# Kernel optimization log

Hardware: AMD Instinct MI355X
Metric: run time of the kernel (lower is better)

Reference implementation:

```python
import jax, jax.numpy as jnp
import numpy as np

N, E, D = 100000, 640000, 128  # nodes, edges, feature dim (in_dim == out_dim == 128)
BN_EPS = 1e-5


def setup_inputs() -> dict:
    key = jax.random.key(0)
    ks = jax.random.split(key, 8)
    x = jax.random.normal(ks[0], (N, D), dtype=jnp.float32)
    edge_index = jax.random.randint(ks[1], (2, E), 0, N, dtype=jnp.int64)
    s = 1.0 / np.sqrt(D)
    W1 = jax.random.uniform(ks[2], (D, D), jnp.float32, -s, s)
    b1 = jax.random.uniform(ks[3], (D,), jnp.float32, -s, s)
    W2 = jax.random.uniform(ks[4], (D, D), jnp.float32, -s, s)
    b2 = jax.random.uniform(ks[5], (D,), jnp.float32, -s, s)
    return {
        "x": x,
        "edge_index": edge_index,
        "eps": jnp.array([0.1], dtype=jnp.float32),
        "W1": W1, "b1": b1,
        "g1": jnp.ones((D,), jnp.float32), "beta1": jnp.zeros((D,), jnp.float32),
        "W2": W2, "b2": b2,
        "g2": jnp.ones((D,), jnp.float32), "beta2": jnp.zeros((D,), jnp.float32),
    }


def _batchnorm(h, gamma, beta):
    # BatchNorm1d in training mode: biased batch stats over the node dim
    mean = jnp.mean(h, axis=0)
    var = jnp.var(h, axis=0)
    return gamma * (h - mean) * jax.lax.rsqrt(var + BN_EPS) + beta


def reference(x, edge_index, eps, W1, b1, g1, beta1, W2, b2, g2, beta2):
    src, dst = edge_index[0], edge_index[1]
    # gather messages from source nodes, scatter-add into destination nodes
    aggr = jax.ops.segment_sum(x[src], dst, num_segments=x.shape[0])  # [N, D]
    h = (1.0 + eps) * x + aggr
    h = jax.nn.relu(_batchnorm(h @ W1.T + b1, g1, beta1))
    h = jax.nn.relu(_batchnorm(h @ W2.T + b2, g2, beta2))
    return h
```

## Files before the change

kernel.cpp:

```cpp
#include <hip/hip_runtime.h>

#define NN 100000
#define DD 128
#define EE 640000
#define NPAD 100352
#define NCHUNK 391
#define NREP 8

typedef __bf16 bf16x8 __attribute__((ext_vector_type(8)));
typedef float floatx4 __attribute__((ext_vector_type(4)));

union BF8 {
    bf16x8 v;
    unsigned short u[8];
    int4 i4;
};

__device__ __forceinline__ unsigned short f2bf(float f) {
    unsigned int u = __float_as_uint(f);
    u += 0x7FFF + ((u >> 16) & 1);
    return (unsigned short)(u >> 16);
}

__device__ __forceinline__ float bf2f(unsigned short h) {
    return __uint_as_float(((unsigned int)h) << 16);
}

__global__ __launch_bounds__(256) void hist_k(const int* __restrict__ ei,
                                              int* __restrict__ degr) {
    int e = blockIdx.x * 256 + threadIdx.x;
    atomicAdd(&degr[(blockIdx.x & (NREP - 1)) * NPAD + ei[EE + e]], 1);
}

__global__ __launch_bounds__(256) void convert_k(const float4* __restrict__ x4,
                                                 ushort4* __restrict__ xbf) {
    int base = blockIdx.x * 1024 + threadIdx.x;
    float4 v0 = x4[base];
    float4 v1 = x4[base + 256];
    float4 v2 = x4[base + 512];
    float4 v3 = x4[base + 768];
    ushort4 u0, u1, u2, u3;
    u0.x = f2bf(v0.x); u0.y = f2bf(v0.y); u0.z = f2bf(v0.z); u0.w = f2bf(v0.w);
    u1.x = f2bf(v1.x); u1.y = f2bf(v1.y); u1.z = f2bf(v1.z); u1.w = f2bf(v1.w);
    u2.x = f2bf(v2.x); u2.y = f2bf(v2.y); u2.z = f2bf(v2.z); u2.w = f2bf(v2.w);
    u3.x = f2bf(v3.x); u3.y = f2bf(v3.y); u3.z = f2bf(v3.z); u3.w = f2bf(v3.w);
    xbf[base] = u0;
    xbf[base + 256] = u1;
    xbf[base + 512] = u2;
    xbf[base + 768] = u3;
}

__global__ __launch_bounds__(256) void scanlb_k(
    int* __restrict__ degr, unsigned int* __restrict__ descr,
    int* __restrict__ offs, int* __restrict__ curr) {
    __shared__ int s[256];
    __shared__ int sbase;
    const int c = blockIdx.x, t = threadIdx.x;
    int g = c * 256 + t;
    int dr[NREP];
    int v = 0;
    if (g < NN) {
#pragma unroll
        for (int r = 0; r < NREP; ++r) {
            dr[r] = degr[r * NPAD + g];
            v += dr[r];
        }
    } else {
#pragma unroll
        for (int r = 0; r < NREP; ++r) dr[r] = 0;
    }
    s[t] = v;
    __syncthreads();
    for (int off = 1; off < 256; off <<= 1) {
        int u = (t >= off) ? s[t - off] : 0;
        __syncthreads();
        s[t] += u;
        __syncthreads();
    }
    const int total = s[255];
    if (c == 0) {
        if (t == 0) {
            __hip_atomic_store(&descr[0], (2u << 30) | (unsigned)total,
                               __ATOMIC_RELEASE, __HIP_MEMORY_SCOPE_AGENT);
            sbase = 0;
        }
    } else if (t < 64) {
        if (t == 0)
            __hip_atomic_store(&descr[c], (1u << 30) | (unsigned)total,
                               __ATOMIC_RELEASE, __HIP_MEMORY_SCOPE_AGENT);
        int acc = 0;
        int base = c - 1;
        while (true) {
            int p = base - t;
            unsigned st = (p >= 0)
                ? __hip_atomic_load(&descr[p], __ATOMIC_ACQUIRE,
                                    __HIP_MEMORY_SCOPE_AGENT)
                : (2u << 30);
            unsigned fl = st >> 30;
            unsigned long long b2 = __ballot(fl == 2u);
            unsigned long long b0 = __ballot(fl == 0u);
            int l2 = b2 ? (__ffsll(b2) - 1) : 64;
            int l0 = b0 ? (__ffsll(b0) - 1) : 64;
            if (l0 < l2) continue;
            unsigned contrib = (t <= l2) ? (st & 0x3FFFFFFFu) : 0u;
#pragma unroll
            for (int o2 = 32; o2 > 0; o2 >>= 1)
                contrib += __shfl_down(contrib, o2, 64);
            contrib = __shfl(contrib, 0, 64);
            acc += (int)contrib;
            if (l2 < 64) break;
            base -= 64;
        }
        if (t == 0) {
            sbase = acc;
            __hip_atomic_store(&descr[c], (2u << 30) | (unsigned)(acc + total),
                               __ATOMIC_RELEASE, __HIP_MEMORY_SCOPE_AGENT);
        }
    }
    __syncthreads();
    if (g < NN) {
        int o = sbase + s[t] - v;
        offs[g] = o;
        int running = o;
#pragma unroll
        for (int r = 0; r < NREP; ++r) {
            curr[r * NPAD + g] = running;
            running += dr[r];
        }
        degr[g] = v;
    }
}

__global__ __launch_bounds__(256) void esort_k(
    const int* __restrict__ ei, int* __restrict__ curr,
    int* __restrict__ ssrc, const float* __restrict__ W1,
    const float* __restrict__ W2, unsigned short* __restrict__ wbf,
    float* __restrict__ stats) {
    int b = blockIdx.x;
    if (b >= 2500) {
        int i = (b - 2500) * 256 + threadIdx.x;
        if (b == 2500) {
            stats[threadIdx.x] = 0.f;
            stats[256 + threadIdx.x] = 0.f;
        }
        const float4* s4 = (i < 4096) ? (const float4*)W1 : (const float4*)W2;
        float4 v = s4[i & 4095];
        ushort4 u;
        u.x = f2bf(v.x); u.y = f2bf(v.y); u.z = f2bf(v.z); u.w = f2bf(v.w);
        ((ushort4*)wbf)[i] = u;
        return;
    }
    int e = b * 256 + threadIdx.x;
    int pos = atomicAdd(&curr[(b & (NREP - 1)) * NPAD + ei[EE + e]], 1);
    ssrc[pos] = ei[e];
}

__global__ __launch_bounds__(256, 4) void aggregate_k(
    const ushort4* __restrict__ xb, const int* __restrict__ ssrc,
    const int* __restrict__ offs, const int* __restrict__ deg,
    const float* __restrict__ epsp, ushort4* __restrict__ hout) {
    int tid = blockIdx.x * 256 + threadIdx.x;
    int node = tid >> 5, lane = tid & 31;
    if (node >= NN) return;
    int start = offs[node], d = deg[node];
    float ef = 1.0f + epsp[0];
    ushort4 ov = xb[node * 32 + lane];
    float ax = ef * bf2f(ov.x), ay = ef * bf2f(ov.y);
    float az = ef * bf2f(ov.z), aw = ef * bf2f(ov.w);
    for (int j = 0; j < d; j += 8) {
        int r = d - j;
        int b = start + j;
        int s0 = ssrc[b];
        int s1 = ssrc[b + ((r > 1) ? 1 : 0)];
        int s2 = ssrc[b + ((r > 2) ? 2 : 0)];
        int s3 = ssrc[b + ((r > 3) ? 3 : 0)];
        int s4i = ssrc[b + ((r > 4) ? 4 : 0)];
        int s5 = ssrc[b + ((r > 5) ? 5 : 0)];
        int s6 = ssrc[b + ((r > 6) ? 6 : 0)];
        int s7 = ssrc[b + ((r > 7) ? 7 : 0)];
        ushort4 x0 = xb[s0 * 32 + lane];
        ushort4 x1 = xb[s1 * 32 + lane];
        ushort4 x2 = xb[s2 * 32 + lane];
        ushort4 x3 = xb[s3 * 32 + lane];
        ushort4 x4v = xb[s4i * 32 + lane];
        ushort4 x5 = xb[s5 * 32 + lane];
        ushort4 x6 = xb[s6 * 32 + lane];
        ushort4 x7 = xb[s7 * 32 + lane];
        float m1 = (r > 1) ? 1.f : 0.f;
        float m2 = (r > 2) ? 1.f : 0.f;
        float m3 = (r > 3) ? 1.f : 0.f;
        float m4 = (r > 4) ? 1.f : 0.f;
        float m5 = (r > 5) ? 1.f : 0.f;
        float m6 = (r > 6) ? 1.f : 0.f;
        float m7 = (r > 7) ? 1.f : 0.f;
        ax += bf2f(x0.x); ay += bf2f(x0.y); az += bf2f(x0.z); aw += bf2f(x0.w);
        ax += m1 * bf2f(x1.x); ay += m1 * bf2f(x1.y); az += m1 * bf2f(x1.z); aw += m1 * bf2f(x1.w);
        ax += m2 * bf2f(x2.x); ay += m2 * bf2f(x2.y); az += m2 * bf2f(x2.z); aw += m2 * bf2f(x2.w);
        ax += m3 * bf2f(x3.x); ay += m3 * bf2f(x3.y); az += m3 * bf2f(x3.z); aw += m3 * bf2f(x3.w);
        ax += m4 * bf2f(x4v.x); ay += m4 * bf2f(x4v.y); az += m4 * bf2f(x4v.z); aw += m4 * bf2f(x4v.w);
        ax += m5 * bf2f(x5.x); ay += m5 * bf2f(x5.y); az += m5 * bf2f(x5.z); aw += m5 * bf2f(x5.w);
        ax += m6 * bf2f(x6.x); ay += m6 * bf2f(x6.y); az += m6 * bf2f(x6.z); aw += m6 * bf2f(x6.w);
        ax += m7 * bf2f(x7.x); ay += m7 * bf2f(x7.y); az += m7 * bf2f(x7.z); aw += m7 * bf2f(x7.w);
    }
    ushort4 u;
    u.x = f2bf(ax); u.y = f2bf(ay); u.z = f2bf(az); u.w = f2bf(aw);
    hout[node * 32 + lane] = u;
}

template <int FUSE_BN, int OUT_BF16>
__global__ __launch_bounds__(256, 2) void gin_gemm_k(
    const unsigned short* __restrict__ hin,
    const float* __restrict__ statsIn,
    const float* __restrict__ gmm,
    const float* __restrict__ bta,
    const unsigned short* __restrict__ Wbf, const float* __restrict__ bias,
    float* __restrict__ yf, unsigned short* __restrict__ yh,
    float* __restrict__ statsOut) {
    __shared__ __align__(16) float s_sum[128];
    __shared__ __align__(16) float s_sq[128];
    __shared__ __align__(16) float sc[128];
    __shared__ __align__(16) float sh[128];
    __shared__ __align__(16) float yst[4][16][132];

    const int tid = threadIdx.x;
    const int l = tid & 63, w = tid >> 6;
    const int m = l & 15, q = l >> 4;

    if (tid < 128) {
        s_sum[tid] = 0.f;
        s_sq[tid] = 0.f;
        if (FUSE_BN) {
            const float inv = 1.0f / (float)NN;
            float mean = statsIn[tid] * inv;
            float var = statsIn[128 + tid] * inv - mean * mean;
            float s = gmm[tid] * rsqrtf(var + 1e-5f);
            sc[tid] = s;
            sh[tid] = bta[tid] - mean * s;
        }
    }

    bf16x8 wf[8][4];
#pragma unroll
    for (int ct = 0; ct < 8; ++ct) {
        const unsigned short* wr = Wbf + (size_t)(ct * 16 + m) * 128 + q * 8;
#pragma unroll
        for (int kc = 0; kc < 4; ++kc) {
            BF8 t;
            t.i4 = *(const int4*)(wr + kc * 32);
            wf[ct][kc] = t.v;
        }
    }
    float bc[8];
#pragma unroll
    for (int ct = 0; ct < 8; ++ct) bc[ct] = bias[ct * 16 + m];

    float ps[8], pq[8];
#pragma unroll
    for (int ct = 0; ct < 8; ++ct) { ps[ct] = 0.f; pq[ct] = 0.f; }

    __syncthreads();

    const int NT = NN / 16;
    const int stride = gridDim.x * 4;
    int t = blockIdx.x * 4 + w;

    const unsigned short* abase = hin + (size_t)m * 128 + q * 8;

    int4 ra[4];
    if (t < NT) {
        const unsigned short* ap = abase + (size_t)t * (16 * 128);
#pragma unroll
        for (int kc = 0; kc < 4; ++kc) ra[kc] = *(const int4*)(ap + kc * 32);
    }

    unsigned short* ysth = (unsigned short*)&yst[w][0][0];

    while (t < NT) {
        bf16x8 a[4];
#pragma unroll
        for (int kc = 0; kc < 4; ++kc) {
            if (FUSE_BN) {
                BF8 raw;
                raw.i4 = ra[kc];
                const float* scp = sc + kc * 32 + q * 8;
                const float* shp = sh + kc * 32 + q * 8;
                float4 s0 = *(const float4*)scp;
                float4 s1 = *(const float4*)(scp + 4);
                float4 h0 = *(const float4*)shp;
                float4 h1 = *(const float4*)(shp + 4);
                BF8 tt;
                tt.u[0] = f2bf(fmaxf(bf2f(raw.u[0]) * s0.x + h0.x, 0.f));
                tt.u[1] = f2bf(fmaxf(bf2f(raw.u[1]) * s0.y + h0.y, 0.f));
                tt.u[2] = f2bf(fmaxf(bf2f(raw.u[2]) * s0.z + h0.z, 0.f));
                tt.u[3] = f2bf(fmaxf(bf2f(raw.u[3]) * s0.w + h0.w, 0.f));
                tt.u[4] = f2bf(fmaxf(bf2f(raw.u[4]) * s1.x + h1.x, 0.f));
                tt.u[5] = f2bf(fmaxf(bf2f(raw.u[5]) * s1.y + h1.y, 0.f));
                tt.u[6] = f2bf(fmaxf(bf2f(raw.u[6]) * s1.z + h1.z, 0.f));
                tt.u[7] = f2bf(fmaxf(bf2f(raw.u[7]) * s1.w + h1.w, 0.f));
                a[kc] = tt.v;
            } else {
                BF8 tt;
                tt.i4 = ra[kc];
                a[kc] = tt.v;
            }
        }

        int tn = t + stride;
        if (tn < NT) {
            const unsigned short* ap = abase + (size_t)tn * (16 * 128);
#pragma unroll
            for (int kc = 0; kc < 4; ++kc) ra[kc] = *(const int4*)(ap + kc * 32);
        }

        floatx4 acc[8];
#pragma unroll
        for (int ct = 0; ct < 8; ++ct) acc[ct] = (floatx4)0.0f;
#pragma unroll
        for (int kc = 0; kc < 4; ++kc)
#pragma unroll
            for (int ct = 0; ct < 8; ++ct)
                acc[ct] = __builtin_amdgcn_mfma_f32_16x16x32_bf16(a[kc], wf[ct][kc], acc[ct], 0, 0, 0);

#pragma unroll
        for (int ct = 0; ct < 8; ++ct) {
#pragma unroll
            for (int i = 0; i < 4; ++i) {
                float yv = acc[ct][i] + bc[ct];
                if (OUT_BF16) {
                    ysth[(q * 4 + i) * 144 + ct * 16 + m] = f2bf(yv);
                } else {
                    yst[w][q * 4 + i][ct * 16 + m] = yv;
                }
                ps[ct] += yv;
                pq[ct] += yv * yv;
            }
        }
        asm volatile("s_waitcnt lgkmcnt(0)" ::: "memory");
        if (OUT_BF16) {
            unsigned short* yb = yh + (size_t)t * (16 * 128);
#pragma unroll
            for (int it = 0; it < 4; ++it) {
                int f = it * 64 + l;
                int row = f >> 4, c8 = f & 15;
                int4 vv = *(const int4*)&ysth[row * 144 + c8 * 8];
                *(int4*)(yb + row * 128 + c8 * 8) = vv;
            }
        } else {
            float* yb = yf + (size_t)t * (16 * 128);
#pragma unroll
            for (int it = 0; it < 8; ++it) {
                int f4 = it * 64 + l;
                int row = f4 >> 5, c4 = f4 & 31;
                float4 vv = *(const float4*)&yst[w][row][c4 * 4];
                *(float4*)(yb + row * 128 + c4 * 4) = vv;
            }
        }
        t = tn;
    }

#pragma unroll
    for (int ct = 0; ct < 8; ++ct) {
        atomicAdd(&s_sum[ct * 16 + m], ps[ct]);
        atomicAdd(&s_sq[ct * 16 + m], pq[ct]);
    }
    __syncthreads();
    if (tid < 128) {
        unsafeAtomicAdd(&statsOut[tid], s_sum[tid]);
        unsafeAtomicAdd(&statsOut[128 + tid], s_sq[tid]);
    }
}

__global__ __launch_bounds__(256) void bn_relu_k(
    const float* __restrict__ y, const float* __restrict__ stats,
    const float* __restrict__ g, const float* __restrict__ beta,
    float* __restrict__ outf) {
    __shared__ __align__(16) float sc[128];
    __shared__ __align__(16) float sh[128];
    int t = threadIdx.x;
    if (t < 128) {
        const float inv = 1.0f / (float)NN;
        float mean = stats[t] * inv;
        float var = stats[128 + t] * inv - mean * mean;
        float s = g[t] * rsqrtf(var + 1e-5f);
        sc[t] = s;
        sh[t] = beta[t] - mean * s;
    }
    __syncthreads();
    const int total4 = NN * 32;
    const float4* y4 = (const float4*)y;
    for (int i = blockIdx.x * 256 + t; i < total4; i += gridDim.x * 256) {
        int c4 = i & 31;
        float4 v = y4[i];
        float4 s = ((const float4*)sc)[c4];
        float4 b = ((const float4*)sh)[c4];
        float r0 = fmaxf(v.x * s.x + b.x, 0.f);
        float r1 = fmaxf(v.y * s.y + b.y, 0.f);
        float r2 = fmaxf(v.z * s.z + b.z, 0.f);
        float r3 = fmaxf(v.w * s.w + b.w, 0.f);
        ((float4*)outf)[i] = make_float4(r0, r1, r2, r3);
    }
}

extern "C" void kernel_launch(void* const* d_in, const int* in_sizes, int n_in,
                              void* d_out, int out_size, void* d_ws, size_t ws_size,
                              hipStream_t stream) {
    const float* x   = (const float*)d_in[0];
    const int* ei    = (const int*)d_in[1];
    const float* eps = (const float*)d_in[2];
    const float* W1  = (const float*)d_in[3];
    const float* b1  = (const float*)d_in[4];
    const float* g1  = (const float*)d_in[5];
    const float* be1 = (const float*)d_in[6];
    const float* W2  = (const float*)d_in[7];
    const float* b2  = (const float*)d_in[8];
    const float* g2  = (const float*)d_in[9];
    const float* be2 = (const float*)d_in[10];
    float* out = (float*)d_out;

    int* degr           = (int*)d_ws;
    unsigned int* descr = (unsigned int*)(degr + NREP * NPAD);
    int* offs           = (int*)(descr + 512);
    int* curr           = offs + NPAD;
    int* ssrc           = curr + NREP * NPAD;
    unsigned short* hbuf = (unsigned short*)(ssrc + EE + 256);
    unsigned short* y1bf = hbuf + (size_t)NN * DD;
    float* stats        = (float*)(y1bf + (size_t)NN * DD);
    unsigned short* wbf = (unsigned short*)(stats + 512);
    ushort4* xbf        = (ushort4*)y1bf;

    hipMemsetAsync(degr, 0, (NREP * NPAD + 512) * sizeof(int), stream);

    hist_k<<<2500, 256, 0, stream>>>(ei, degr);
    convert_k<<<3125, 256, 0, stream>>>((const float4*)x, xbf);
    scanlb_k<<<NCHUNK, 256, 0, stream>>>(degr, descr, offs, curr);
    esort_k<<<2500 + 32, 256, 0, stream>>>(ei, curr, ssrc, W1, W2, wbf, stats);
    aggregate_k<<<(NN * 32 + 255) / 256, 256, 0, stream>>>(
        xbf, ssrc, offs, degr, eps, (ushort4*)hbuf);

    const int gblocks = 512;
    gin_gemm_k<0, 1><<<gblocks, 256, 0, stream>>>(
        hbuf, nullptr, nullptr, nullptr, wbf, b1, nullptr, y1bf, stats);
    gin_gemm_k<1, 0><<<gblocks, 256, 0, stream>>>(
        y1bf, stats, g1, be1, wbf + 16384, b2, out, nullptr, stats + 256);
    bn_relu_k<<<4096, 256, 0, stream>>>(out, stats + 256, g2, be2, out);
}
```

Before: 310.4 us.

## Fold x conversion into esort launch and store second GEMM output as bf16

The fp32-to-bf16 conversion of x moves out of its own kernel and into extra blocks of the edge-sort kernel, which removes one launch and lets the conversion overlap with the scatter work. The second GEMM now writes its pre-BN result as bf16 into a scratch buffer instead of fp32 into the output. The final BN+ReLU pass reads that bf16 buffer and writes fp32, which cuts memory traffic for the intermediate. The risk is extra rounding error, since batch-norm statistics are computed in fp32 but normalisation is applied to bf16-rounded values.

```diff
diff --git a/kernel.cpp b/kernel.cpp
--- a/kernel.cpp
+++ b/kernel.cpp
@@ -30,24 +30,6 @@
                                               int* __restrict__ degr) {
     int e = blockIdx.x * 256 + threadIdx.x;
     atomicAdd(&degr[(blockIdx.x & (NREP - 1)) * NPAD + ei[EE + e]], 1);
-}
-
-__global__ __launch_bounds__(256) void convert_k(const float4* __restrict__ x4,
-                                                 ushort4* __restrict__ xbf) {
-    int base = blockIdx.x * 1024 + threadIdx.x;
-    float4 v0 = x4[base];
-    float4 v1 = x4[base + 256];
-    float4 v2 = x4[base + 512];
-    float4 v3 = x4[base + 768];
-    ushort4 u0, u1, u2, u3;
-    u0.x = f2bf(v0.x); u0.y = f2bf(v0.y); u0.z = f2bf(v0.z); u0.w = f2bf(v0.w);
-    u1.x = f2bf(v1.x); u1.y = f2bf(v1.y); u1.z = f2bf(v1.z); u1.w = f2bf(v1.w);
-    u2.x = f2bf(v2.x); u2.y = f2bf(v2.y); u2.z = f2bf(v2.z); u2.w = f2bf(v2.w);
-    u3.x = f2bf(v3.x); u3.y = f2bf(v3.y); u3.z = f2bf(v3.z); u3.w = f2bf(v3.w);
-    xbf[base] = u0;
-    xbf[base + 256] = u1;
-    xbf[base + 512] = u2;
-    xbf[base + 768] = u3;
 }
 
 __global__ __launch_bounds__(256) void scanlb_k(
@@ -135,8 +117,26 @@
     const int* __restrict__ ei, int* __restrict__ curr,
     int* __restrict__ ssrc, const float* __restrict__ W1,
     const float* __restrict__ W2, unsigned short* __restrict__ wbf,
-    float* __restrict__ stats) {
+    float* __restrict__ stats, const float4* __restrict__ x4,
+    ushort4* __restrict__ xbf) {
     int b = blockIdx.x;
+    if (b >= 2532) {
+        int base = (b - 2532) * 1024 + threadIdx.x;
+        float4 v0 = x4[base];
+        float4 v1 = x4[base + 256];
+        float4 v2 = x4[base + 512];
+        float4 v3 = x4[base + 768];
+        ushort4 u0, u1, u2, u3;
+        u0.x = f2bf(v0.x); u0.y = f2bf(v0.y); u0.z = f2bf(v0.z); u0.w = f2bf(v0.w);
+        u1.x = f2bf(v1.x); u1.y = f2bf(v1.y); u1.z = f2bf(v1.z); u1.w = f2bf(v1.w);
+        u2.x = f2bf(v2.x); u2.y = f2bf(v2.y); u2.z = f2bf(v2.z); u2.w = f2bf(v2.w);
+        u3.x = f2bf(v3.x); u3.y = f2bf(v3.y); u3.z = f2bf(v3.z); u3.w = f2bf(v3.w);
+        xbf[base] = u0;
+        xbf[base + 256] = u1;
+        xbf[base + 512] = u2;
+        xbf[base + 768] = u3;
+        return;
+    }
     if (b >= 2500) {
         int i = (b - 2500) * 256 + threadIdx.x;
         if (b == 2500) {
@@ -371,9 +371,9 @@
 }
 
 __global__ __launch_bounds__(256) void bn_relu_k(
-    const float* __restrict__ y, const float* __restrict__ stats,
+    const ushort4* __restrict__ yh, const float* __restrict__ stats,
     const float* __restrict__ g, const float* __restrict__ beta,
-    float* __restrict__ outf) {
+    float4* __restrict__ outf) {
     __shared__ __align__(16) float sc[128];
     __shared__ __align__(16) float sh[128];
     int t = threadIdx.x;
@@ -387,17 +387,16 @@
     }
     __syncthreads();
     const int total4 = NN * 32;
-    const float4* y4 = (const float4*)y;
     for (int i = blockIdx.x * 256 + t; i < total4; i += gridDim.x * 256) {
         int c4 = i & 31;
-        float4 v = y4[i];
+        ushort4 v = yh[i];
         float4 s = ((const float4*)sc)[c4];
         float4 b = ((const float4*)sh)[c4];
-        float r0 = fmaxf(v.x * s.x + b.x, 0.f);
-        float r1 = fmaxf(v.y * s.y + b.y, 0.f);
-        float r2 = fmaxf(v.z * s.z + b.z, 0.f);
-        float r3 = fmaxf(v.w * s.w + b.w, 0.f);
-        ((float4*)outf)[i] = make_float4(r0, r1, r2, r3);
+        float r0 = fmaxf(bf2f(v.x) * s.x + b.x, 0.f);
+        float r1 = fmaxf(bf2f(v.y) * s.y + b.y, 0.f);
+        float r2 = fmaxf(bf2f(v.z) * s.z + b.z, 0.f);
+        float r3 = fmaxf(bf2f(v.w) * s.w + b.w, 0.f);
+        outf[i] = make_float4(r0, r1, r2, r3);
     }
 }
 
@@ -431,16 +430,17 @@
     hipMemsetAsync(degr, 0, (NREP * NPAD + 512) * sizeof(int), stream);
 
     hist_k<<<2500, 256, 0, stream>>>(ei, degr);
-    convert_k<<<3125, 256, 0, stream>>>((const float4*)x, xbf);
     scanlb_k<<<NCHUNK, 256, 0, stream>>>(degr, descr, offs, curr);
-    esort_k<<<2500 + 32, 256, 0, stream>>>(ei, curr, ssrc, W1, W2, wbf, stats);
+    esort_k<<<2500 + 32 + 3125, 256, 0, stream>>>(
+        ei, curr, ssrc, W1, W2, wbf, stats, (const float4*)x, xbf);
     aggregate_k<<<(NN * 32 + 255) / 256, 256, 0, stream>>>(
         xbf, ssrc, offs, degr, eps, (ushort4*)hbuf);
 
     const int gblocks = 512;
     gin_gemm_k<0, 1><<<gblocks, 256, 0, stream>>>(
         hbuf, nullptr, nullptr, nullptr, wbf, b1, nullptr, y1bf, stats);
-    gin_gemm_k<1, 0><<<gblocks, 256, 0, stream>>>(
-        y1bf, stats, g1, be1, wbf + 16384, b2, out, nullptr, stats + 256);
-    bn_relu_k<<<4096, 256, 0, stream>>>(out, stats + 256, g2, be2, out);
-}
+    gin_gemm_k<1, 1><<<gblocks, 256, 0, stream>>>(
+        y1bf, stats, g1, be1, wbf + 16384, b2, nullptr, hbuf, stats + 256);
+    bn_relu_k<<<4096, 256, 0, stream>>>(
+        (const ushort4*)hbuf, stats + 256, g2, be2, (float4*)out);
+}
```

Result: no change. 306.0 us (-1.4%).
